# Optimization experiments

Measured on AMD Instinct MI355X. Metric: run time of the kernel, lower is better.

Reference implementation:

```python
import jax, jax.numpy as jnp
import numpy as np

ALPHA = 0.2  # LeakyReLU negative slope
NEG_BIG = -9e15


def setup_inputs() -> dict:
    key = jax.random.key(0)
    k1, k2, k3, k4 = jax.random.split(key, 4)
    B, N, Fin, Fout = 16, 1024, 256, 256
    h = jax.random.normal(k1, (B, N, Fin), dtype=jnp.float32)
    adj = jax.random.randint(k2, (B, N, N), 0, 2, dtype=jnp.int32)
    # xavier_uniform with gain=1.414
    def xavier(k, shape, gain=1.414):
        fan_in, fan_out = shape[0], shape[1]
        bound = gain * np.sqrt(6.0 / (fan_in + fan_out))
        return jax.random.uniform(k, shape, jnp.float32, -bound, bound)
    W = xavier(k3, (Fin, Fout))
    a = xavier(k4, (2 * Fout, 1))
    return {"h": h, "adj": adj, "W": W, "a": a}


def reference(h, adj, W, a):
    # h: [B,N,Fin], adj: [B,N,N], W: [Fin,Fout], a: [2*Fout,1]
    Fout = W.shape[1]
    Wh = jnp.einsum('bnf,fo->bno', h, W)                      # [B,N,Fout]
    a1, a2 = a[:Fout, 0], a[Fout:, 0]                          # [Fout], [Fout]
    # e_ij = leakyrelu(Wh_i . a1 + Wh_j . a2) -- outer sum, no O(N^2*F) tensor
    f1 = Wh @ a1                                               # [B,N]
    f2 = Wh @ a2                                               # [B,N]
    e = jax.nn.leaky_relu(f1[:, :, None] + f2[:, None, :], negative_slope=ALPHA)
    attention = jnp.where(adj > 0, e, jnp.float32(NEG_BIG))    # [B,N,N]
    attention = jax.nn.softmax(attention, axis=2)
    h_prime = jnp.einsum('bij,bjo->bio', attention, Wh)        # [B,N,Fout]
    return jax.nn.elu(h_prime)
```

## Files before the change

kernel.cpp:

```cpp
#include <hip/hip_runtime.h>
#include <hip/hip_bf16.h>

#define Bsz 16
#define Nn  1024
#define Ff  256
#define ALPHA 0.2f
#define NEG_BIG -9.0e15f

typedef __attribute__((ext_vector_type(8))) short short8;
typedef __attribute__((ext_vector_type(4))) float f32x4;
typedef __attribute__((ext_vector_type(4))) unsigned short ushort4_t;

__device__ __forceinline__ unsigned short f2bf(float x) {
    union { __hip_bfloat16 b; unsigned short u; } cv;
    cv.b = __float2bfloat16(x);
    return cv.u;
}

__global__ __launch_bounds__(256) void gat_prep(
    const float* __restrict__ W, const float* __restrict__ a,
    float* __restrict__ w1, float* __restrict__ w2)
{
    const int t = threadIdx.x, w = t >> 6, ln = t & 63;
    __shared__ float a1s[Ff], a2s[Ff];
    a1s[t] = a[t];
    a2s[t] = a[Ff + t];
    __syncthreads();
    const int f = blockIdx.x * 4 + w;
    float s1 = 0.f, s2 = 0.f;
    #pragma unroll
    for (int c = 0; c < 4; c++) {
        const int o = ln + 64 * c;
        const float wv = W[(size_t)f * Ff + o];
        s1 += wv * a1s[o];
        s2 += wv * a2s[o];
    }
    #pragma unroll
    for (int off = 1; off < 64; off <<= 1) {
        s1 += __shfl_xor(s1, off, 64);
        s2 += __shfl_xor(s2, off, 64);
    }
    if (ln == 0) { w1[f] = s1; w2[f] = s2; }
}

__global__ __launch_bounds__(256) void pack_f(
    const float* __restrict__ h, const float* __restrict__ W,
    const float* __restrict__ w1, const float* __restrict__ w2,
    unsigned short* __restrict__ hK, unsigned short* __restrict__ WK,
    float* __restrict__ f1, float* __restrict__ f2)
{
    __shared__ float tile[32][257];
    const int id = blockIdx.x, t = threadIdx.x, w = t >> 6, ln = t & 63;
    const bool isH = (id < 512);
    const float* src;
    unsigned short* dst;
    int grow0 = 0;
    if (isH) {
        const int b = id >> 5, kt = id & 31;
        grow0 = b * Nn + kt * 32;
        src = h + (size_t)grow0 * Ff;
        dst = hK + ((size_t)(b * 32 + kt)) * 8192;
    } else {
        const int ft = id - 512;
        src = W + (size_t)ft * 32 * Ff;
        dst = WK + (size_t)ft * 8192;
    }
    #pragma unroll
    for (int rr = 0; rr < 8; rr++) {
        const int row = rr * 4 + w;
        const int col = ln * 4;
        const float4 v = *(const float4*)&src[row * Ff + col];
        tile[row][col] = v.x; tile[row][col + 1] = v.y;
        tile[row][col + 2] = v.z; tile[row][col + 3] = v.w;
    }
    __syncthreads();

    unsigned* d32 = (unsigned*)dst;
    #pragma unroll
    for (int k = 0; k < 16; k++) {
        const int fidx = k * 256 + t;
        const int o = fidx >> 4, q = fidx & 15;
        const unsigned lo = f2bf(tile[2 * q][o]);
        const unsigned hi = f2bf(tile[2 * q + 1][o]);
        d32[fidx] = lo | (hi << 16);
    }

    if (isH) {
        float w1r[4], w2r[4];
        #pragma unroll
        for (int c = 0; c < 4; c++) {
            w1r[c] = w1[ln + 64 * c];
            w2r[c] = w2[ln + 64 * c];
        }
        #pragma unroll
        for (int rr = 0; rr < 8; rr++) {
            const int row = rr * 4 + w;
            float s1 = 0.f, s2 = 0.f;
            #pragma unroll
            for (int c = 0; c < 4; c++) {
                const float hv = tile[row][ln + 64 * c];
                s1 += hv * w1r[c];
                s2 += hv * w2r[c];
            }
            #pragma unroll
            for (int off = 1; off < 64; off <<= 1) {
                s1 += __shfl_xor(s1, off, 64);
                s2 += __shfl_xor(s2, off, 64);
            }
            if (ln == 0) { f1[grow0 + row] = s1; f2[grow0 + row] = s2; }
        }
    }
}

#define TI 32
__global__ __launch_bounds__(512, 4) void gat_attn(
    const int* __restrict__ adj,
    const float* __restrict__ f1, const float* __restrict__ f2,
    const unsigned short* __restrict__ hK, const unsigned short* __restrict__ WK,
    float* __restrict__ out)
{
    __shared__ unsigned short pbf[TI * 1024];
    const int t = threadIdx.x, w = t >> 6, ln = t & 63;
    const int m = ln & 15, quad = ln >> 4;
    const int bid = blockIdx.x;
    const int b  = 2 * (bid & 7) + ((bid >> 3) & 1);
    const int i0 = (bid >> 4) * TI;

    float4 f2r[4];
    #pragma unroll
    for (int c = 0; c < 4; c++)
        f2r[c] = *(const float4*)&f2[b * Nn + 256 * c + 4 * ln];

    const int grb = b * Nn + i0 + w * 4;
    const int* aptr = adj + (size_t)grb * Nn;
    int4 av0[4], av1[4];
    #pragma unroll
    for (int c = 0; c < 4; c++) {
        av0[c] = *(const int4*)&aptr[c * 256 + 4 * ln];
        av1[c] = *(const int4*)&aptr[Nn + c * 256 + 4 * ln];
    }
    #pragma unroll
    for (int p = 0; p < 2; p++) {
        int4 nv0[4], nv1[4];
        if (p == 0) {
            #pragma unroll
            for (int c = 0; c < 4; c++) {
                nv0[c] = *(const int4*)&aptr[2 * Nn + c * 256 + 4 * ln];
                nv1[c] = *(const int4*)&aptr[3 * Nn + c * 256 + 4 * ln];
            }
        }
        const int r0 = w * 4 + 2 * p, r1 = r0 + 1;
        const float fi0 = f1[grb + 2 * p], fi1 = f1[grb + 2 * p + 1];
        float e0[16], e1[16];
        float mx0 = -INFINITY, mx1 = -INFINITY;
        #pragma unroll
        for (int c = 0; c < 4; c++) {
            const float4 fv = f2r[c];
            float x;
            x = fi0 + fv.x; x = x > 0.f ? x : ALPHA * x; x = av0[c].x > 0 ? x : NEG_BIG; e0[4*c+0] = x; mx0 = fmaxf(mx0, x);
            x = fi0 + fv.y; x = x > 0.f ? x : ALPHA * x; x = av0[c].y > 0 ? x : NEG_BIG; e0[4*c+1] = x; mx0 = fmaxf(mx0, x);
            x = fi0 + fv.z; x = x > 0.f ? x : ALPHA * x; x = av0[c].z > 0 ? x : NEG_BIG; e0[4*c+2] = x; mx0 = fmaxf(mx0, x);
            x = fi0 + fv.w; x = x > 0.f ? x : ALPHA * x; x = av0[c].w > 0 ? x : NEG_BIG; e0[4*c+3] = x; mx0 = fmaxf(mx0, x);
            x = fi1 + fv.x; x = x > 0.f ? x : ALPHA * x; x = av1[c].x > 0 ? x : NEG_BIG; e1[4*c+0] = x; mx1 = fmaxf(mx1, x);
            x = fi1 + fv.y; x = x > 0.f ? x : ALPHA * x; x = av1[c].y > 0 ? x : NEG_BIG; e1[4*c+1] = x; mx1 = fmaxf(mx1, x);
            x = fi1 + fv.z; x = x > 0.f ? x : ALPHA * x; x = av1[c].z > 0 ? x : NEG_BIG; e1[4*c+2] = x; mx1 = fmaxf(mx1, x);
            x = fi1 + fv.w; x = x > 0.f ? x : ALPHA * x; x = av1[c].w > 0 ? x : NEG_BIG; e1[4*c+3] = x; mx1 = fmaxf(mx1, x);
        }
        #pragma unroll
        for (int off = 1; off < 64; off <<= 1) {
            mx0 = fmaxf(mx0, __shfl_xor(mx0, off, 64));
            mx1 = fmaxf(mx1, __shfl_xor(mx1, off, 64));
        }
        float s0 = 0.f, s1 = 0.f;
        #pragma unroll
        for (int c = 0; c < 16; c++) {
            e0[c] = __expf(e0[c] - mx0); s0 += e0[c];
            e1[c] = __expf(e1[c] - mx1); s1 += e1[c];
        }
        #pragma unroll
        for (int off = 1; off < 64; off <<= 1) {
            s0 += __shfl_xor(s0, off, 64);
            s1 += __shfl_xor(s1, off, 64);
        }
        const float ri0 = 1.f / s0, ri1 = 1.f / s1;
        #pragma unroll
        for (int c = 0; c < 4; c++) {
            const int j = 256 * c + 4 * ln;
            ushort4_t v0 = { f2bf(e0[4*c] * ri0), f2bf(e0[4*c+1] * ri0),
                             f2bf(e0[4*c+2] * ri0), f2bf(e0[4*c+3] * ri0) };
            ushort4_t v1 = { f2bf(e1[4*c] * ri1), f2bf(e1[4*c+1] * ri1),
                             f2bf(e1[4*c+2] * ri1), f2bf(e1[4*c+3] * ri1) };
            *(ushort4_t*)&pbf[r0 * 1024 + (j ^ ((r0 & 7) << 3))] = v0;
            *(ushort4_t*)&pbf[r1 * 1024 + (j ^ ((r1 & 7) << 3))] = v1;
        }
        #pragma unroll
        for (int c = 0; c < 4; c++) { av0[c] = nv0[c]; av1[c] = nv1[c]; }
    }
    __syncthreads();

    const int n0 = w * 32;
    const unsigned short* hKb = hK + (size_t)b * 32 * 8192;
    const int arow0 = m * 1024, arow1 = (16 + m) * 1024;
    const int asw = (m & 7) << 3;
    #define AF0(kt) (*(const short8*)&pbf[arow0 + ((((kt) * 32) + quad * 8) ^ asw)])
    #define AF1(kt) (*(const short8*)&pbf[arow1 + ((((kt) * 32) + quad * 8) ^ asw)])
    #define BF0(kt) (*(const short8*)&hKb[(size_t)(kt) * 8192 + (n0 + m) * 32 + quad * 8])
    #define BF1(kt) (*(const short8*)&hKb[(size_t)(kt) * 8192 + (n0 + 16 + m) * 32 + quad * 8])

    f32x4 acc00 = {0.f,0.f,0.f,0.f}, acc01 = acc00, acc10 = acc00, acc11 = acc00;
    short8 a0c = AF0(0), a1c = AF1(0);
    short8 b0c = BF0(0), b1c = BF1(0);
    short8 b0n = BF0(1), b1n = BF1(1);
    #pragma unroll
    for (int kt = 0; kt < 32; kt++) {
        short8 b0nn = b0c, b1nn = b1c, a0n = a0c, a1n = a1c;
        if (kt + 2 < 32) { b0nn = BF0(kt + 2); b1nn = BF1(kt + 2); }
        if (kt + 1 < 32) { a0n = AF0(kt + 1); a1n = AF1(kt + 1); }
        acc00 = __builtin_amdgcn_mfma_f32_16x16x32_bf16(a0c, b0c, acc00, 0, 0, 0);
        acc01 = __builtin_amdgcn_mfma_f32_16x16x32_bf16(a0c, b1c, acc01, 0, 0, 0);
        acc10 = __builtin_amdgcn_mfma_f32_16x16x32_bf16(a1c, b0c, acc10, 0, 0, 0);
        acc11 = __builtin_amdgcn_mfma_f32_16x16x32_bf16(a1c, b1c, acc11, 0, 0, 0);
        a0c = a0n; a1c = a1n; b0c = b0n; b1c = b1n; b0n = b0nn; b1n = b1nn;
    }

    __syncthreads();
    #pragma unroll
    for (int reg = 0; reg < 4; reg++) {
        pbf[(quad * 4 + reg) * 264 + n0 + m]           = f2bf(acc00[reg]);
        pbf[(quad * 4 + reg) * 264 + n0 + 16 + m]      = f2bf(acc01[reg]);
        pbf[(16 + quad * 4 + reg) * 264 + n0 + m]      = f2bf(acc10[reg]);
        pbf[(16 + quad * 4 + reg) * 264 + n0 + 16 + m] = f2bf(acc11[reg]);
    }
    __syncthreads();

    #define GA0(kt) (*(const short8*)&pbf[m * 264 + (kt) * 32 + quad * 8])
    #define GA1(kt) (*(const short8*)&pbf[(16 + m) * 264 + (kt) * 32 + quad * 8])
    #define WB0(kt) (*(const short8*)&WK[(size_t)(kt) * 8192 + (n0 + m) * 32 + quad * 8])
    #define WB1(kt) (*(const short8*)&WK[(size_t)(kt) * 8192 + (n0 + 16 + m) * 32 + quad * 8])

    f32x4 c00 = {0.f,0.f,0.f,0.f}, c01 = c00, c10 = c00, c11 = c00;
    short8 ga0 = GA0(0), ga1 = GA1(0);
    short8 wb0 = WB0(0), wb1 = WB1(0);
    #pragma unroll
    for (int kt = 0; kt < 8; kt++) {
        short8 ga0n = ga0, ga1n = ga1, wb0n = wb0, wb1n = wb1;
        if (kt + 1 < 8) { ga0n = GA0(kt+1); ga1n = GA1(kt+1); wb0n = WB0(kt+1); wb1n = WB1(kt+1); }
        c00 = __builtin_amdgcn_mfma_f32_16x16x32_bf16(ga0, wb0, c00, 0, 0, 0);
        c01 = __builtin_amdgcn_mfma_f32_16x16x32_bf16(ga0, wb1, c01, 0, 0, 0);
        c10 = __builtin_amdgcn_mfma_f32_16x16x32_bf16(ga1, wb0, c10, 0, 0, 0);
        c11 = __builtin_amdgcn_mfma_f32_16x16x32_bf16(ga1, wb1, c11, 0, 0, 0);
        ga0 = ga0n; ga1 = ga1n; wb0 = wb0n; wb1 = wb1n;
    }
    const size_t ob = (size_t)(b * Nn) + i0;
    #pragma unroll
    for (int reg = 0; reg < 4; reg++) {
        float v;
        v = c00[reg]; v = v > 0.f ? v : (__expf(v) - 1.f);
        out[(ob + quad * 4 + reg) * Ff + n0 + m] = v;
        v = c01[reg]; v = v > 0.f ? v : (__expf(v) - 1.f);
        out[(ob + quad * 4 + reg) * Ff + n0 + 16 + m] = v;
        v = c10[reg]; v = v > 0.f ? v : (__expf(v) - 1.f);
        out[(ob + 16 + quad * 4 + reg) * Ff + n0 + m] = v;
        v = c11[reg]; v = v > 0.f ? v : (__expf(v) - 1.f);
        out[(ob + 16 + quad * 4 + reg) * Ff + n0 + 16 + m] = v;
    }
}

extern "C" void kernel_launch(void* const* d_in, const int* in_sizes, int n_in,
                              void* d_out, int out_size, void* d_ws, size_t ws_size,
                              hipStream_t stream)
{
    const void* h   = d_in[0];
    const void* adj = d_in[1];
    const void* W   = d_in[2];
    const void* a   = d_in[3];
    for (int i = 0; i < n_in; i++) {
        if      (in_sizes[i] == Bsz * Nn * Ff) h   = d_in[i];
        else if (in_sizes[i] == Bsz * Nn * Nn) adj = d_in[i];
        else if (in_sizes[i] == Ff * Ff)       W   = d_in[i];
        else if (in_sizes[i] == 2 * Ff)        a   = d_in[i];
    }
    float* out = (float*)d_out;

    char*  wsb = (char*)d_ws;
    float* w1  = (float*)wsb;
    float* w2  = w1 + Ff;
    float* f1  = (float*)(wsb + 4096);
    float* f2  = f1 + Bsz * Nn;
    unsigned short* hK = (unsigned short*)(wsb + 4096 + 2 * 65536);
    unsigned short* WK = hK + (size_t)Bsz * 32 * 8192;

    gat_prep<<<64, 256, 0, stream>>>((const float*)W, (const float*)a, w1, w2);
    pack_f<<<520, 256, 0, stream>>>((const float*)h, (const float*)W, w1, w2, hK, WK, f1, f2);
    gat_attn<<<Bsz * (Nn / TI), 512, 0, stream>>>((const int*)adj, f1, f2, hK, WK, out);
}
```

Before: 142.1 us.

## Use 1024-thread blocks in gat_attn with one row pair and 16 columns per wave

```diff
diff --git a/kernel.cpp b/kernel.cpp
--- a/kernel.cpp
+++ b/kernel.cpp
@@ -49,7 +49,7 @@
     unsigned short* __restrict__ hK, unsigned short* __restrict__ WK,
     float* __restrict__ f1, float* __restrict__ f2)
 {
-    __shared__ float tile[32][257];
+    __shared__ __align__(16) float tile[32][260];
     const int id = blockIdx.x, t = threadIdx.x, w = t >> 6, ln = t & 63;
     const bool isH = (id < 512);
     const float* src;
@@ -69,9 +69,7 @@
     for (int rr = 0; rr < 8; rr++) {
         const int row = rr * 4 + w;
         const int col = ln * 4;
-        const float4 v = *(const float4*)&src[row * Ff + col];
-        tile[row][col] = v.x; tile[row][col + 1] = v.y;
-        tile[row][col + 2] = v.z; tile[row][col + 3] = v.w;
+        *(float4*)&tile[row][col] = *(const float4*)&src[row * Ff + col];
     }
     __syncthreads();
 
@@ -113,13 +111,13 @@
 }
 
 #define TI 32
-__global__ __launch_bounds__(512, 4) void gat_attn(
+__global__ __launch_bounds__(1024, 8) void gat_attn(
     const int* __restrict__ adj,
     const float* __restrict__ f1, const float* __restrict__ f2,
     const unsigned short* __restrict__ hK, const unsigned short* __restrict__ WK,
     float* __restrict__ out)
 {
-    __shared__ unsigned short pbf[TI * 1024];
+    __shared__ __align__(16) unsigned short pbf[TI * 1024];
     const int t = threadIdx.x, w = t >> 6, ln = t & 63;
     const int m = ln & 15, quad = ln >> 4;
     const int bid = blockIdx.x;
@@ -131,7 +129,8 @@
     for (int c = 0; c < 4; c++)
         f2r[c] = *(const float4*)&f2[b * Nn + 256 * c + 4 * ln];
 
-    const int grb = b * Nn + i0 + w * 4;
+    const int r0 = 2 * w, r1 = r0 + 1;
+    const int grb = b * Nn + i0 + r0;
     const int* aptr = adj + (size_t)grb * Nn;
     int4 av0[4], av1[4];
     #pragma unroll
@@ -139,130 +138,106 @@
         av0[c] = *(const int4*)&aptr[c * 256 + 4 * ln];
         av1[c] = *(const int4*)&aptr[Nn + c * 256 + 4 * ln];
     }
-    #pragma unroll
-    for (int p = 0; p < 2; p++) {
-        int4 nv0[4], nv1[4];
-        if (p == 0) {
-            #pragma unroll
-            for (int c = 0; c < 4; c++) {
-                nv0[c] = *(const int4*)&aptr[2 * Nn + c * 256 + 4 * ln];
-                nv1[c] = *(const int4*)&aptr[3 * Nn + c * 256 + 4 * ln];
-            }
-        }
-        const int r0 = w * 4 + 2 * p, r1 = r0 + 1;
-        const float fi0 = f1[grb + 2 * p], fi1 = f1[grb + 2 * p + 1];
-        float e0[16], e1[16];
-        float mx0 = -INFINITY, mx1 = -INFINITY;
-        #pragma unroll
-        for (int c = 0; c < 4; c++) {
-            const float4 fv = f2r[c];
-            float x;
-            x = fi0 + fv.x; x = x > 0.f ? x : ALPHA * x; x = av0[c].x > 0 ? x : NEG_BIG; e0[4*c+0] = x; mx0 = fmaxf(mx0, x);
-            x = fi0 + fv.y; x = x > 0.f ? x : ALPHA * x; x = av0[c].y > 0 ? x : NEG_BIG; e0[4*c+1] = x; mx0 = fmaxf(mx0, x);
-            x = fi0 + fv.z; x = x > 0.f ? x : ALPHA * x; x = av0[c].z > 0 ? x : NEG_BIG; e0[4*c+2] = x; mx0 = fmaxf(mx0, x);
-            x = fi0 + fv.w; x = x > 0.f ? x : ALPHA * x; x = av0[c].w > 0 ? x : NEG_BIG; e0[4*c+3] = x; mx0 = fmaxf(mx0, x);
-            x = fi1 + fv.x; x = x > 0.f ? x : ALPHA * x; x = av1[c].x > 0 ? x : NEG_BIG; e1[4*c+0] = x; mx1 = fmaxf(mx1, x);
-            x = fi1 + fv.y; x = x > 0.f ? x : ALPHA * x; x = av1[c].y > 0 ? x : NEG_BIG; e1[4*c+1] = x; mx1 = fmaxf(mx1, x);
-            x = fi1 + fv.z; x = x > 0.f ? x : ALPHA * x; x = av1[c].z > 0 ? x : NEG_BIG; e1[4*c+2] = x; mx1 = fmaxf(mx1, x);
-            x = fi1 + fv.w; x = x > 0.f ? x : ALPHA * x; x = av1[c].w > 0 ? x : NEG_BIG; e1[4*c+3] = x; mx1 = fmaxf(mx1, x);
-        }
-        #pragma unroll
-        for (int off = 1; off < 64; off <<= 1) {
-            mx0 = fmaxf(mx0, __shfl_xor(mx0, off, 64));
-            mx1 = fmaxf(mx1, __shfl_xor(mx1, off, 64));
-        }
-        float s0 = 0.f, s1 = 0.f;
-        #pragma unroll
-        for (int c = 0; c < 16; c++) {
-            e0[c] = __expf(e0[c] - mx0); s0 += e0[c];
-            e1[c] = __expf(e1[c] - mx1); s1 += e1[c];
-        }
-        #pragma unroll
-        for (int off = 1; off < 64; off <<= 1) {
-            s0 += __shfl_xor(s0, off, 64);
-            s1 += __shfl_xor(s1, off, 64);
-        }
-        const float ri0 = 1.f / s0, ri1 = 1.f / s1;
-        #pragma unroll
-        for (int c = 0; c < 4; c++) {
-            const int j = 256 * c + 4 * ln;
-            ushort4_t v0 = { f2bf(e0[4*c] * ri0), f2bf(e0[4*c+1] * ri0),
-                             f2bf(e0[4*c+2] * ri0), f2bf(e0[4*c+3] * ri0) };
-            ushort4_t v1 = { f2bf(e1[4*c] * ri1), f2bf(e1[4*c+1] * ri1),
-                             f2bf(e1[4*c+2] * ri1), f2bf(e1[4*c+3] * ri1) };
-            *(ushort4_t*)&pbf[r0 * 1024 + (j ^ ((r0 & 7) << 3))] = v0;
-            *(ushort4_t*)&pbf[r1 * 1024 + (j ^ ((r1 & 7) << 3))] = v1;
-        }
-        #pragma unroll
-        for (int c = 0; c < 4; c++) { av0[c] = nv0[c]; av1[c] = nv1[c]; }
-    }
-    __syncthreads();
-
-    const int n0 = w * 32;
+    const float fi0 = f1[grb], fi1 = f1[grb + 1];
+    float e0[16], e1[16];
+    float mx0 = -INFINITY, mx1 = -INFINITY;
+    #pragma unroll
+    for (int c = 0; c < 4; c++) {
+        const float4 fv = f2r[c];
+        float x, y;
+        x = fi0 + fv.x; x = fmaxf(x, ALPHA * x); x = av0[c].x > 0 ? x : NEG_BIG; e0[4*c+0] = x;
+        y = fi0 + fv.y; y = fmaxf(y, ALPHA * y); y = av0[c].y > 0 ? y : NEG_BIG; e0[4*c+1] = y;
+        mx0 = fmaxf(fmaxf(x, y), mx0);
+        x = fi0 + fv.z; x = fmaxf(x, ALPHA * x); x = av0[c].z > 0 ? x : NEG_BIG; e0[4*c+2] = x;
+        y = fi0 + fv.w; y = fmaxf(y, ALPHA * y); y = av0[c].w > 0 ? y : NEG_BIG; e0[4*c+3] = y;
+        mx0 = fmaxf(fmaxf(x, y), mx0);
+        x = fi1 + fv.x; x = fmaxf(x, ALPHA * x); x = av1[c].x > 0 ? x : NEG_BIG; e1[4*c+0] = x;
+        y = fi1 + fv.y; y = fmaxf(y, ALPHA * y); y = av1[c].y > 0 ? y : NEG_BIG; e1[4*c+1] = y;
+        mx1 = fmaxf(fmaxf(x, y), mx1);
+        x = fi1 + fv.z; x = fmaxf(x, ALPHA * x); x = av1[c].z > 0 ? x : NEG_BIG; e1[4*c+2] = x;
+        y = fi1 + fv.w; y = fmaxf(y, ALPHA * y); y = av1[c].w > 0 ? y : NEG_BIG; e1[4*c+3] = y;
+        mx1 = fmaxf(fmaxf(x, y), mx1);
+    }
+    #pragma unroll
+    for (int off = 1; off < 64; off <<= 1) {
+        mx0 = fmaxf(mx0, __shfl_xor(mx0, off, 64));
+        mx1 = fmaxf(mx1, __shfl_xor(mx1, off, 64));
+    }
+    float s0 = 0.f, s1 = 0.f;
+    #pragma unroll
+    for (int c = 0; c < 16; c++) {
+        e0[c] = __expf(e0[c] - mx0); s0 += e0[c];
+        e1[c] = __expf(e1[c] - mx1); s1 += e1[c];
+    }
+    #pragma unroll
+    for (int off = 1; off < 64; off <<= 1) {
+        s0 += __shfl_xor(s0, off, 64);
+        s1 += __shfl_xor(s1, off, 64);
+    }
+    const float ri0 = 1.f / s0, ri1 = 1.f / s1;
+    #pragma unroll
+    for (int c = 0; c < 4; c++) {
+        const int j = 256 * c + 4 * ln;
+        ushort4_t v0 = { f2bf(e0[4*c] * ri0), f2bf(e0[4*c+1] * ri0),
+                         f2bf(e0[4*c+2] * ri0), f2bf(e0[4*c+3] * ri0) };
+        ushort4_t v1 = { f2bf(e1[4*c] * ri1), f2bf(e1[4*c+1] * ri1),
+                         f2bf(e1[4*c+2] * ri1), f2bf(e1[4*c+3] * ri1) };
+        *(ushort4_t*)&pbf[r0 * 1024 + (j ^ ((r0 & 7) << 3))] = v0;
+        *(ushort4_t*)&pbf[r1 * 1024 + (j ^ ((r1 & 7) << 3))] = v1;
+    }
+    __syncthreads();
+
+    const int n0 = w * 16;
     const unsigned short* hKb = hK + (size_t)b * 32 * 8192;
     const int arow0 = m * 1024, arow1 = (16 + m) * 1024;
     const int asw = (m & 7) << 3;
     #define AF0(kt) (*(const short8*)&pbf[arow0 + ((((kt) * 32) + quad * 8) ^ asw)])
     #define AF1(kt) (*(const short8*)&pbf[arow1 + ((((kt) * 32) + quad * 8) ^ asw)])
-    #define BF0(kt) (*(const short8*)&hKb[(size_t)(kt) * 8192 + (n0 + m) * 32 + quad * 8])
-    #define BF1(kt) (*(const short8*)&hKb[(size_t)(kt) * 8192 + (n0 + 16 + m) * 32 + quad * 8])
-
-    f32x4 acc00 = {0.f,0.f,0.f,0.f}, acc01 = acc00, acc10 = acc00, acc11 = acc00;
+    #define BF(kt)  (*(const short8*)&hKb[(size_t)(kt) * 8192 + (n0 + m) * 32 + quad * 8])
+
+    f32x4 acc0 = {0.f,0.f,0.f,0.f}, acc1 = acc0;
     short8 a0c = AF0(0), a1c = AF1(0);
-    short8 b0c = BF0(0), b1c = BF1(0);
-    short8 b0n = BF0(1), b1n = BF1(1);
+    short8 bc = BF(0), bn = BF(1);
     #pragma unroll
     for (int kt = 0; kt < 32; kt++) {
-        short8 b0nn = b0c, b1nn = b1c, a0n = a0c, a1n = a1c;
-        if (kt + 2 < 32) { b0nn = BF0(kt + 2); b1nn = BF1(kt + 2); }
+        short8 bnn = bc, a0n = a0c, a1n = a1c;
+        if (kt + 2 < 32) bnn = BF(kt + 2);
         if (kt + 1 < 32) { a0n = AF0(kt + 1); a1n = AF1(kt + 1); }
-        acc00 = __builtin_amdgcn_mfma_f32_16x16x32_bf16(a0c, b0c, acc00, 0, 0, 0);
-        acc01 = __builtin_amdgcn_mfma_f32_16x16x32_bf16(a0c, b1c, acc01, 0, 0, 0);
-        acc10 = __builtin_amdgcn_mfma_f32_16x16x32_bf16(a1c, b0c, acc10, 0, 0, 0);
-        acc11 = __builtin_amdgcn_mfma_f32_16x16x32_bf16(a1c, b1c, acc11, 0, 0, 0);
-        a0c = a0n; a1c = a1n; b0c = b0n; b1c = b1n; b0n = b0nn; b1n = b1nn;
+        acc0 = __builtin_amdgcn_mfma_f32_16x16x32_bf16(a0c, bc, acc0, 0, 0, 0);
+        acc1 = __builtin_amdgcn_mfma_f32_16x16x32_bf16(a1c, bc, acc1, 0, 0, 0);
+        a0c = a0n; a1c = a1n; bc = bn; bn = bnn;
     }
 
     __syncthreads();
     #pragma unroll
     for (int reg = 0; reg < 4; reg++) {
-        pbf[(quad * 4 + reg) * 264 + n0 + m]           = f2bf(acc00[reg]);
-        pbf[(quad * 4 + reg) * 264 + n0 + 16 + m]      = f2bf(acc01[reg]);
-        pbf[(16 + quad * 4 + reg) * 264 + n0 + m]      = f2bf(acc10[reg]);
-        pbf[(16 + quad * 4 + reg) * 264 + n0 + 16 + m] = f2bf(acc11[reg]);
+        pbf[(quad * 4 + reg) * 264 + n0 + m]      = f2bf(acc0[reg]);
+        pbf[(16 + quad * 4 + reg) * 264 + n0 + m] = f2bf(acc1[reg]);
     }
     __syncthreads();
 
     #define GA0(kt) (*(const short8*)&pbf[m * 264 + (kt) * 32 + quad * 8])
     #define GA1(kt) (*(const short8*)&pbf[(16 + m) * 264 + (kt) * 32 + quad * 8])
-    #define WB0(kt) (*(const short8*)&WK[(size_t)(kt) * 8192 + (n0 + m) * 32 + quad * 8])
-    #define WB1(kt) (*(const short8*)&WK[(size_t)(kt) * 8192 + (n0 + 16 + m) * 32 + quad * 8])
-
-    f32x4 c00 = {0.f,0.f,0.f,0.f}, c01 = c00, c10 = c00, c11 = c00;
-    short8 ga0 = GA0(0), ga1 = GA1(0);
-    short8 wb0 = WB0(0), wb1 = WB1(0);
+    #define WB(kt)  (*(const short8*)&WK[(size_t)(kt) * 8192 + (n0 + m) * 32 + quad * 8])
+
+    f32x4 c0 = {0.f,0.f,0.f,0.f}, c1 = c0;
+    short8 ga0 = GA0(0), ga1 = GA1(0), wb = WB(0);
     #pragma unroll
     for (int kt = 0; kt < 8; kt++) {
-        short8 ga0n = ga0, ga1n = ga1, wb0n = wb0, wb1n = wb1;
-        if (kt + 1 < 8) { ga0n = GA0(kt+1); ga1n = GA1(kt+1); wb0n = WB0(kt+1); wb1n = WB1(kt+1); }
-        c00 = __builtin_amdgcn_mfma_f32_16x16x32_bf16(ga0, wb0, c00, 0, 0, 0);
-        c01 = __builtin_amdgcn_mfma_f32_16x16x32_bf16(ga0, wb1, c01, 0, 0, 0);
-        c10 = __builtin_amdgcn_mfma_f32_16x16x32_bf16(ga1, wb0, c10, 0, 0, 0);
-        c11 = __builtin_amdgcn_mfma_f32_16x16x32_bf16(ga1, wb1, c11, 0, 0, 0);
-        ga0 = ga0n; ga1 = ga1n; wb0 = wb0n; wb1 = wb1n;
+        short8 ga0n = ga0, ga1n = ga1, wbn = wb;
+        if (kt + 1 < 8) { ga0n = GA0(kt + 1); ga1n = GA1(kt + 1); wbn = WB(kt + 1); }
+        c0 = __builtin_amdgcn_mfma_f32_16x16x32_bf16(ga0, wb, c0, 0, 0, 0);
+        c1 = __builtin_amdgcn_mfma_f32_16x16x32_bf16(ga1, wb, c1, 0, 0, 0);
+        ga0 = ga0n; ga1 = ga1n; wb = wbn;
     }
     const size_t ob = (size_t)(b * Nn) + i0;
     #pragma unroll
     for (int reg = 0; reg < 4; reg++) {
         float v;
-        v = c00[reg]; v = v > 0.f ? v : (__expf(v) - 1.f);
+        v = c0[reg]; v = v > 0.f ? v : (__expf(v) - 1.f);
         out[(ob + quad * 4 + reg) * Ff + n0 + m] = v;
-        v = c01[reg]; v = v > 0.f ? v : (__expf(v) - 1.f);
-        out[(ob + quad * 4 + reg) * Ff + n0 + 16 + m] = v;
-        v = c10[reg]; v = v > 0.f ? v : (__expf(v) - 1.f);
+        v = c1[reg]; v = v > 0.f ? v : (__expf(v) - 1.f);
         out[(ob + 16 + quad * 4 + reg) * Ff + n0 + m] = v;
-        v = c11[reg]; v = v > 0.f ? v : (__expf(v) - 1.f);
-        out[(ob + 16 + quad * 4 + reg) * Ff + n0 + 16 + m] = v;
     }
 }
 
@@ -292,5 +267,5 @@
 
     gat_prep<<<64, 256, 0, stream>>>((const float*)W, (const float*)a, w1, w2);
     pack_f<<<520, 256, 0, stream>>>((const float*)h, (const float*)W, w1, w2, hK, WK, f1, f2);
-    gat_attn<<<Bsz * (Nn / TI), 512, 0, stream>>>((const int*)adj, f1, f2, hK, WK, out);
-}
+    gat_attn<<<Bsz * (Nn / TI), 1024, 0, stream>>>((const int*)adj, f1, f2, hK, WK, out);
+}
```

Result: faster. 136.7 us (-3.8%).
